# Performance work log

Measured on AMD Instinct MI355X. Metric: run time of the kernel, lower is better.

The kernel has to match this reference:

```python
import jax, jax.numpy as jnp
import numpy as np

B, L, D, H = 48, 512, 192, 6
DK = D // H
HID = 4 * D
EPS = 1e-5
SCALE = 1.0 / np.float32(np.sqrt(DK))


def _ln(x, g, b):
    mu = x.mean(-1, keepdims=True)
    v = ((x - mu) ** 2).mean(-1, keepdims=True)
    return (x - mu) * jax.lax.rsqrt(v + EPS) * g + b


def _mln(x, m, g, b):
    # masked layernorm: valid rows normalized, invalid rows pass through unchanged
    return jnp.where(m[..., None], _ln(x, g, b), x)


def _mha(q, k, v, mask, wq, bq, wk, bk, wv, bv, wo, bo):
    def proj(x, w, bb):
        return (x @ w + bb).reshape(B, L, H, DK).transpose(0, 2, 1, 3)  # [B,H,L,dk]
    Q, K, V = proj(q, wq, bq), proj(k, wk, bk), proj(v, wv, bv)
    s = jnp.einsum('bhqd,bhkd->bhqk', Q, K) * SCALE
    s = jnp.where(mask[:, None], -1e9, s)  # mask True = invalid pair
    p = jax.nn.softmax(s, axis=-1)
    o = jnp.einsum('bhqk,bhkd->bhqd', p, V).transpose(0, 2, 1, 3).reshape(B, L, D)
    return o @ wo + bo


def _forward(x_a, x_b, valid_a, valid_b,
             ln_a_g, ln_a_b, ln_b_g, ln_b_b, ln_oa_g, ln_oa_b, ln_ob_g, ln_ob_b,
             wq, bq, wk, bk, wv, bv, wo, bo,
             fln_g, fln_b, flno_g, flno_b, w1, b1, w2, b2):
    mB2A = ~(valid_a[:, :, None] & valid_b[:, None, :])  # [B,La,Lb]
    mA2B = ~(valid_b[:, :, None] & valid_a[:, None, :])
    a = _mln(x_a, valid_a, ln_a_g, ln_a_b)
    b = _mln(x_b, valid_b, ln_b_g, ln_b_b)
    oa = _mha(a, b, b, mB2A, wq, bq, wk, bk, wv, bv, wo, bo)
    oa = _mln(oa + x_a, valid_a, ln_oa_g, ln_oa_b)
    ob = _mha(b, a, a, mA2B, wq, bq, wk, bk, wv, bv, wo, bo)
    ob = _mln(ob + x_b, valid_b, ln_ob_g, ln_ob_b)

    def ffn(x, m):
        xn = _mln(x, m, fln_g, fln_b)
        y = jax.nn.gelu(xn @ w1 + b1, approximate=False) @ w2 + b2
        return _mln(x + y, m, flno_g, flno_b)

    return ffn(oa, valid_a), ffn(ob, valid_b)


def setup_inputs() -> dict:
    key = jax.random.key(0)
    ks = jax.random.split(key, 12)
    p = lambda k, s: jax.random.normal(k, s, dtype=jnp.float32) * 0.02
    ones = lambda s: jnp.ones(s, dtype=jnp.float32)
    zeros = lambda s: jnp.zeros(s, dtype=jnp.float32)
    return {
        'x_a': jax.random.normal(ks[0], (B, L, D), dtype=jnp.float32),
        'x_b': jax.random.normal(ks[1], (B, L, D), dtype=jnp.float32),
        'valid_a': jax.random.bernoulli(ks[2], 0.9, (B, L)),
        'valid_b': jax.random.bernoulli(ks[3], 0.9, (B, L)),
        'ln_a_g': ones((D,)), 'ln_a_b': zeros((D,)),
        'ln_b_g': ones((D,)), 'ln_b_b': zeros((D,)),
        'ln_oa_g': ones((D,)), 'ln_oa_b': zeros((D,)),
        'ln_ob_g': ones((D,)), 'ln_ob_b': zeros((D,)),
        'wq': p(ks[4], (D, D)), 'bq': zeros((D,)),
        'wk': p(ks[5], (D, D)), 'bk': zeros((D,)),
        'wv': p(ks[6], (D, D)), 'bv': zeros((D,)),
        'wo': p(ks[7], (D, D)), 'bo': zeros((D,)),
        'fln_g': ones((D,)), 'fln_b': zeros((D,)),
        'flno_g': ones((D,)), 'flno_b': zeros((D,)),
        'w1': p(ks[8], (D, HID)), 'b1': zeros((HID,)),
        'w2': p(ks[9], (HID, D)), 'b2': zeros((D,)),
    }


def reference(x_a, x_b, valid_a, valid_b,
              ln_a_g, ln_a_b, ln_b_g, ln_b_b, ln_oa_g, ln_oa_b, ln_ob_g, ln_ob_b,
              wq, bq, wk, bk, wv, bv, wo, bo,
              fln_g, fln_b, flno_g, flno_b, w1, b1, w2, b2):
    return _forward(x_a, x_b, valid_a, valid_b,
                    ln_a_g, ln_a_b, ln_b_g, ln_b_b, ln_oa_g, ln_oa_b, ln_ob_g, ln_ob_b,
                    wq, bq, wk, bk, wv, bv, wo, bo,
                    fln_g, fln_b, flno_g, flno_b, w1, b1, w2, b2)
```

## Files before the change

### kernel.cpp

```cpp
#include <hip/hip_runtime.h>
#include <math.h>

#define BB 48
#define LL 512
#define DD 192
#define HH 6
#define DKK 32
#define HID 768
#define ROWS (BB * LL)
#define BLD ((size_t)ROWS * DD)
#define SB2 0.25503531f
#define MASKED_X (-36.0f)

typedef unsigned short ushort_t;
typedef unsigned int uint_t;
typedef __bf16 bf16x8 __attribute__((ext_vector_type(8)));
typedef float f32x4 __attribute__((ext_vector_type(4)));

union U4BF8 { uint4 u; bf16x8 b; };
union BFU { __bf16 h; ushort_t u; };

__device__ __forceinline__ ushort_t f2bf(float f) {
  union { float f; uint_t u; } v; v.f = f;
  uint_t r = v.u + 0x7fffu + ((v.u >> 16) & 1u);
  return (ushort_t)(r >> 16);
}
__device__ __forceinline__ ushort_t cvt_bf(float f) {
  BFU c; c.h = (__bf16)f; return c.u;
}

__device__ __forceinline__ int swz_w(int n, int k, int N) {
  return ((k >> 5) * (N >> 4) + (n >> 4)) * 512 +
         ((((k & 31) >> 3) << 4) + (n & 15)) * 8 + (k & 7);
}

__global__ __launch_bounds__(256) void pack_kernel(
    const float* __restrict__ wq, const float* __restrict__ wk,
    const float* __restrict__ wv, const float* __restrict__ wo,
    const float* __restrict__ w1, const float* __restrict__ w2,
    const float* __restrict__ bq, const float* __restrict__ bk,
    const float* __restrict__ bv,
    ushort_t* __restrict__ Wqkv, ushort_t* __restrict__ Wo,
    ushort_t* __restrict__ W1, ushort_t* __restrict__ W2,
    float* __restrict__ bqkv) {
  int i = blockIdx.x * 256 + threadIdx.x;
  if (i < 110592) {
    int n2 = i / 192, k = i - n2 * 192;
    int part = n2 / 192, n = n2 - part * 192;
    const float* src = part == 0 ? wq : (part == 1 ? wk : wv);
    Wqkv[swz_w(n2, k, 576)] = f2bf(src[k * 192 + n]);
  } else if (i < 147456) {
    int j = i - 110592;
    int n = j / 192, k = j - n * 192;
    Wo[swz_w(n, k, 192)] = f2bf(wo[k * 192 + n]);
  } else if (i < 294912) {
    int j = i - 147456;
    int n = j / 192, k = j - n * 192;
    W1[j] = f2bf(w1[k * 768 + n]);
  } else if (i < 442368) {
    int j = i - 294912;
    int n = j / 768, k = j - n * 768;
    W2[j] = f2bf(w2[k * 192 + n]);
  } else if (i < 442944) {
    int j = i - 442368;
    bqkv[j] = j < 192 ? bq[j] : (j < 384 ? bk[j - 192] : bv[j - 384]);
  }
}

__global__ __launch_bounds__(256) void qkv_ln_kernel(
    const float* __restrict__ xa, const float* __restrict__ xb,
    const int* __restrict__ va, const int* __restrict__ vb,
    const float* __restrict__ g_a, const float* __restrict__ b_a,
    const float* __restrict__ g_b, const float* __restrict__ b_b,
    const ushort_t* __restrict__ Wsw, const float* __restrict__ bias,
    ushort_t* __restrict__ Cb) {
  constexpr int N = 576;
  constexpr int CSB = N + 8;
  __shared__ ushort_t smem[32 * CSB];
  ushort_t* As = smem;

  int tid = threadIdx.x;
  int w = tid >> 6, lane = tid & 63, l15 = lane & 15, kq = lane >> 4;
  int row0 = blockIdx.x * 32;
  int side = row0 >= ROWS;
  int rb = row0 - side * ROWS;

  {
    int row = tid >> 3, l8 = tid & 7;
    const float* xr = (side ? xb : xa) + (size_t)(rb + row) * DD + l8 * 24;
    float v[24];
    float s = 0.f;
#pragma unroll
    for (int j = 0; j < 6; ++j) {
      float4 q = *(const float4*)(xr + j * 4);
      v[j*4+0] = q.x; v[j*4+1] = q.y; v[j*4+2] = q.z; v[j*4+3] = q.w;
      s += q.x + q.y + q.z + q.w;
    }
    s += __shfl_xor(s, 1); s += __shfl_xor(s, 2); s += __shfl_xor(s, 4);
    float mu = s * (1.0f / 192.0f);
    float ss = 0.f;
#pragma unroll
    for (int j = 0; j < 24; ++j) { float d = v[j] - mu; ss += d * d; }
    ss += __shfl_xor(ss, 1); ss += __shfl_xor(ss, 2); ss += __shfl_xor(ss, 4);
    float inv = rsqrtf(ss * (1.0f / 192.0f) + 1e-5f);
    int vld = (side ? vb : va)[rb + row];
    const float* g = side ? g_b : g_a;
    const float* be = side ? b_b : b_a;
    ushort_t ob[24];
#pragma unroll
    for (int j = 0; j < 24; ++j) {
      int col = l8 * 24 + j;
      float r = vld ? (v[j] - mu) * inv * g[col] + be[col] : v[j];
      ob[j] = f2bf(r);
    }
#pragma unroll
    for (int j = 0; j < 3; ++j)
      *(uint4*)(&As[row * 200 + l8 * 24 + j * 8]) = *(const uint4*)(&ob[j * 8]);
  }
  __syncthreads();

  f32x4 acc[2][9];
#pragma unroll
  for (int qs = 0; qs < 2; ++qs)
#pragma unroll
    for (int nt = 0; nt < 9; ++nt) acc[qs][nt] = (f32x4){0.f, 0.f, 0.f, 0.f};

#pragma unroll 1
  for (int kk = 0; kk < 6; ++kk) {
    bf16x8 af[2];
#pragma unroll
    for (int qs = 0; qs < 2; ++qs)
      af[qs] = *(const bf16x8*)(&As[(qs * 16 + l15) * 200 + kk * 32 + kq * 8]);
    const ushort_t* wp =
        Wsw + ((size_t)(kk * (N >> 4) + w * 9) << 9) + lane * 8;
#pragma unroll
    for (int nt = 0; nt < 9; ++nt) {
      U4BF8 wf;
      wf.u = *(const uint4*)(wp + (nt << 9));
#pragma unroll
      for (int qs = 0; qs < 2; ++qs)
        acc[qs][nt] = __builtin_amdgcn_mfma_f32_16x16x32_bf16(
            af[qs], wf.b, acc[qs][nt], 0, 0, 0);
    }
  }
  __syncthreads();

  ushort_t* Cs = smem;
#pragma unroll
  for (int nt = 0; nt < 9; ++nt) {
    int col = (w * 9 + nt) * 16 + l15;
    float bb = bias[col];
#pragma unroll
    for (int qs = 0; qs < 2; ++qs)
#pragma unroll
      for (int r = 0; r < 4; ++r)
        Cs[(qs * 16 + kq * 4 + r) * CSB + col] = f2bf(acc[qs][nt][r] + bb);
  }
  __syncthreads();
  constexpr int UPR = (N * 2) / 16;
#pragma unroll
  for (int i = 0; i < (32 * UPR) / 256; ++i) {
    int idx = tid + i * 256;
    int r = idx / UPR, u = idx - r * UPR;
    *(uint4*)(Cb + (size_t)row0 * N + idx * 8) =
        *(const uint4*)(&Cs[r * CSB + u * 8]);
  }
}

__global__ __launch_bounds__(256) void oproj_ln_kernel(
    const ushort_t* __restrict__ A, const ushort_t* __restrict__ Wsw,
    const float* __restrict__ bias,
    const float* __restrict__ xa, const float* __restrict__ xb,
    const int* __restrict__ va, const int* __restrict__ vb,
    const float* __restrict__ g_oa, const float* __restrict__ b_oa,
    const float* __restrict__ g_ob, const float* __restrict__ b_ob,
    const float* __restrict__ g_f, const float* __restrict__ b_f,
    float* __restrict__ outf, ushort_t* __restrict__ outb) {
  __shared__ float smemf[32 * 196];
  ushort_t* As = (ushort_t*)smemf;

  int tid = threadIdx.x;
  int w = tid >> 6, lane = tid & 63, l15 = lane & 15, kq = lane >> 4;
  int row0 = blockIdx.x * 32;
  int side = row0 >= ROWS;
  int rb = row0 - side * ROWS;

  {
    const ushort_t* ap = A + (size_t)row0 * DD;
#pragma unroll
    for (int i = 0; i < 3; ++i) {
      int idx = tid + i * 256;
      int r = idx / 24, c = (idx - r * 24) * 8;
      *(uint4*)(&As[r * 200 + c]) = *(const uint4*)(ap + idx * 8);
    }
  }
  __syncthreads();

  f32x4 acc[2][3];
#pragma unroll
  for (int qs = 0; qs < 2; ++qs)
#pragma unroll
    for (int nt = 0; nt < 3; ++nt) acc[qs][nt] = (f32x4){0.f, 0.f, 0.f, 0.f};

#pragma unroll 1
  for (int kk = 0; kk < 6; ++kk) {
    bf16x8 af[2];
#pragma unroll
    for (int qs = 0; qs < 2; ++qs)
      af[qs] = *(const bf16x8*)(&As[(qs * 16 + l15) * 200 + kk * 32 + kq * 8]);
    const ushort_t* wp =
        Wsw + ((size_t)(kk * (192 >> 4) + w * 3) << 9) + lane * 8;
#pragma unroll
    for (int nt = 0; nt < 3; ++nt) {
      U4BF8 wf;
      wf.u = *(const uint4*)(wp + (nt << 9));
#pragma unroll
      for (int qs = 0; qs < 2; ++qs)
        acc[qs][nt] = __builtin_amdgcn_mfma_f32_16x16x32_bf16(
            af[qs], wf.b, acc[qs][nt], 0, 0, 0);
    }
  }
  __syncthreads();

  float* Cs = smemf;
#pragma unroll
  for (int nt = 0; nt < 3; ++nt) {
    int col = (w * 3 + nt) * 16 + l15;
    float bb = bias[col];
#pragma unroll
    for (int qs = 0; qs < 2; ++qs)
#pragma unroll
      for (int r = 0; r < 4; ++r)
        Cs[(qs * 16 + kq * 4 + r) * 196 + col] = acc[qs][nt][r] + bb;
  }
  __syncthreads();

  int row = tid >> 3, l8 = tid & 7;
  int grow = row0 + row;
  const float* xrow = (side ? xb : xa) + (size_t)(rb + row) * DD;
  const float* crow = &Cs[row * 196];
  float v[24];
  float s = 0.f;
#pragma unroll
  for (int j = 0; j < 6; ++j) {
    int col = j * 32 + l8 * 4;
    float4 q = *(const float4*)(xrow + col);
    v[j*4+0] = crow[col+0] + q.x; v[j*4+1] = crow[col+1] + q.y;
    v[j*4+2] = crow[col+2] + q.z; v[j*4+3] = crow[col+3] + q.w;
    s += v[j*4+0] + v[j*4+1] + v[j*4+2] + v[j*4+3];
  }
  s += __shfl_xor(s, 1); s += __shfl_xor(s, 2); s += __shfl_xor(s, 4);
  float mu = s * (1.0f / 192.0f);
  float ss = 0.f;
#pragma unroll
  for (int j = 0; j < 24; ++j) { float d = v[j] - mu; ss += d * d; }
  ss += __shfl_xor(ss, 1); ss += __shfl_xor(ss, 2); ss += __shfl_xor(ss, 4);
  float inv = rsqrtf(ss * (1.0f / 192.0f) + 1e-5f);
  int vld = (side ? vb : va)[rb + row];
  const float* g1 = side ? g_ob : g_oa;
  const float* b1 = side ? b_ob : b_oa;
  float y[24];
#pragma unroll
  for (int j = 0; j < 6; ++j) {
#pragma unroll
    for (int e = 0; e < 4; ++e) {
      int col = j * 32 + l8 * 4 + e;
      float vv = v[j * 4 + e];
      y[j * 4 + e] = vld ? (vv - mu) * inv * g1[col] + b1[col] : vv;
    }
  }
  float* orow = outf + (size_t)grow * DD;
#pragma unroll
  for (int j = 0; j < 6; ++j) {
    float4 q = {y[j*4+0], y[j*4+1], y[j*4+2], y[j*4+3]};
    *(float4*)(orow + j * 32 + l8 * 4) = q;
  }
  float s2 = 0.f;
#pragma unroll
  for (int j = 0; j < 24; ++j) s2 += y[j];
  s2 += __shfl_xor(s2, 1); s2 += __shfl_xor(s2, 2); s2 += __shfl_xor(s2, 4);
  float mu2 = s2 * (1.0f / 192.0f);
  float ss2 = 0.f;
#pragma unroll
  for (int j = 0; j < 24; ++j) { float e = y[j] - mu2; ss2 += e * e; }
  ss2 += __shfl_xor(ss2, 1); ss2 += __shfl_xor(ss2, 2); ss2 += __shfl_xor(ss2, 4);
  float inv2 = rsqrtf(ss2 * (1.0f / 192.0f) + 1e-5f);
  ushort_t* obrow = outb + (size_t)grow * DD;
#pragma unroll
  for (int j = 0; j < 6; ++j) {
    ushort_t zb[4];
#pragma unroll
    for (int e = 0; e < 4; ++e) {
      int col = j * 32 + l8 * 4 + e;
      float z = vld ? (y[j*4+e] - mu2) * inv2 * g_f[col] + b_f[col] : y[j*4+e];
      zb[e] = f2bf(z);
    }
    *(uint2*)(obrow + j * 32 + l8 * 4) = *(const uint2*)(&zb[0]);
  }
}

__global__ __launch_bounds__(256, 3) void ffn_fused_kernel(
    const ushort_t* __restrict__ A, const ushort_t* __restrict__ W1t,
    const float* __restrict__ bias1, const ushort_t* __restrict__ W2t,
    const float* __restrict__ bias2,
    const int* __restrict__ va, const int* __restrict__ vb,
    const float* __restrict__ g_f, const float* __restrict__ b_f,
    float* __restrict__ outf) {
  __shared__ float smemf[64 * 196];
  ushort_t* As = (ushort_t*)smemf;
  ushort_t* Hs = As + 64 * 200;

  int tid = threadIdx.x;
  int w = tid >> 6;
  int lane = tid & 63;
  int l15 = lane & 15;
  int kq = lane >> 4;
  int row0 = blockIdx.x * 64;
  int side = row0 >= ROWS;
  int rb0 = row0 - side * ROWS;

#pragma unroll
  for (int i = 0; i < 6; ++i) {
    int idx = tid + i * 256;
    int r = idx / 24, c = (idx % 24) * 8;
    *(uint4*)(&As[r * 200 + c]) = *(const uint4*)(A + (size_t)(row0 + r) * DD + c);
  }

  const ushort_t* w1p = W1t + (size_t)(w * 16 + l15) * DD + kq * 8;
  const ushort_t* w2p = W2t + (size_t)(w * 48 + l15) * HID + kq * 8;

  U4BF8 w1f[6], w1n[6], w2f[6];
#pragma unroll
  for (int kk = 0; kk < 6; ++kk)
    w1f[kk].u = *(const uint4*)(w1p + kk * 32);

  f32x4 Cacc[4][3];
#pragma unroll
  for (int qs = 0; qs < 4; ++qs)
#pragma unroll
    for (int nt = 0; nt < 3; ++nt) Cacc[qs][nt] = (f32x4){0.f, 0.f, 0.f, 0.f};

  __syncthreads();

  for (int hc = 0; hc < 12; ++hc) {
#pragma unroll
    for (int kk2 = 0; kk2 < 2; ++kk2)
#pragma unroll
      for (int nt = 0; nt < 3; ++nt)
        w2f[kk2 * 3 + nt].u =
            *(const uint4*)(w2p + (size_t)(nt * 16) * HID + hc * 64 + kk2 * 32);

    f32x4 Hacc[4];
#pragma unroll
    for (int qs = 0; qs < 4; ++qs) Hacc[qs] = (f32x4){0.f, 0.f, 0.f, 0.f};
#pragma unroll
    for (int kk = 0; kk < 6; ++kk) {
#pragma unroll
      for (int qs = 0; qs < 4; ++qs) {
        bf16x8 af = *(const bf16x8*)(&As[(qs * 16 + l15) * 200 + kk * 32 + kq * 8]);
        Hacc[qs] = __builtin_amdgcn_mfma_f32_16x16x32_bf16(
            af, w1f[kk].b, Hacc[qs], 0, 0, 0);
      }
    }

    if (hc < 11) {
#pragma unroll
      for (int kk = 0; kk < 6; ++kk)
        w1n[kk].u = *(const uint4*)(w1p + (size_t)(hc + 1) * 64 * DD + kk * 32);
    }

    {
      float bb = bias1[hc * 64 + w * 16 + l15];
      ushort_t* hb = &Hs[(hc & 1) * 4608];
#pragma unroll
      for (int qs = 0; qs < 4; ++qs)
#pragma unroll
        for (int r = 0; r < 4; ++r) {
          float x = Hacc[qs][r] + bb;
          x = 0.5f * x * (1.0f + erff(x * 0.70710678118654752f));
          hb[(qs * 16 + kq * 4 + r) * 72 + w * 16 + l15] = f2bf(x);
        }
    }
    __syncthreads();

#pragma unroll
    for (int kk2 = 0; kk2 < 2; ++kk2) {
      bf16x8 hf[4];
#pragma unroll
      for (int qs = 0; qs < 4; ++qs)
        hf[qs] = *(const bf16x8*)(&Hs[(hc & 1) * 4608 +
                                      (qs * 16 + l15) * 72 + kk2 * 32 + kq * 8]);
#pragma unroll
      for (int nt = 0; nt < 3; ++nt)
#pragma unroll
        for (int qs = 0; qs < 4; ++qs)
          Cacc[qs][nt] = __builtin_amdgcn_mfma_f32_16x16x32_bf16(
              hf[qs], w2f[kk2 * 3 + nt].b, Cacc[qs][nt], 0, 0, 0);
    }

#pragma unroll
    for (int kk = 0; kk < 6; ++kk) w1f[kk] = w1n[kk];
  }
  __syncthreads();

  float* Cs = smemf;
#pragma unroll
  for (int qs = 0; qs < 4; ++qs)
#pragma unroll
    for (int nt = 0; nt < 3; ++nt) {
      int col = w * 48 + nt * 16 + l15;
      float bb = bias2[col];
#pragma unroll
      for (int r = 0; r < 4; ++r)
        Cs[(qs * 16 + kq * 4 + r) * 196 + col] = Cacc[qs][nt][r] + bb;
    }
  __syncthreads();

  int row = tid >> 2, l4 = tid & 3;
  int grow = row0 + row;
  float* orow = outf + (size_t)grow * DD;
  const float* crow = &Cs[row * 196];
  float v[48];
  float s = 0.f;
#pragma unroll
  for (int j = 0; j < 12; ++j) {
    int col = j * 16 + l4 * 4;
    float4 q = *(const float4*)(orow + col);
    v[j*4+0] = crow[col+0] + q.x; v[j*4+1] = crow[col+1] + q.y;
    v[j*4+2] = crow[col+2] + q.z; v[j*4+3] = crow[col+3] + q.w;
    s += v[j*4+0] + v[j*4+1] + v[j*4+2] + v[j*4+3];
  }
  s += __shfl_xor(s, 1); s += __shfl_xor(s, 2);
  float mu = s * (1.0f / 192.0f);
  float ss = 0.f;
#pragma unroll
  for (int j = 0; j < 48; ++j) { float d = v[j] - mu; ss += d * d; }
  ss += __shfl_xor(ss, 1); ss += __shfl_xor(ss, 2);
  float inv = rsqrtf(ss * (1.0f / 192.0f) + 1e-5f);
  int vld = (side ? vb : va)[rb0 + row];
#pragma unroll
  for (int j = 0; j < 12; ++j) {
    int col = j * 16 + l4 * 4;
    float4 q;
#pragma unroll
    for (int e = 0; e < 4; ++e) {
      float vv = v[j * 4 + e];
      ((float*)&q)[e] = vld ? (vv - mu) * inv * g_f[col + e] + b_f[col + e] : vv;
    }
    *(float4*)(orow + col) = q;
  }
}

__global__ __launch_bounds__(256) void attn_mfma_kernel(
    const ushort_t* __restrict__ QKV,
    const int* __restrict__ valid_a, const int* __restrict__ valid_b,
    ushort_t* __restrict__ out) {
  int i = blockIdx.x;
  int gid = ((i >> 5) << 3) | (i & 7);
  int qt = (i >> 3) & 3;
  int side = gid >= BB * HH;
  int grem = side ? gid - BB * HH : gid;
  int h = grem % HH;
  int batch = grem / HH;
  int tid = threadIdx.x;
  int w = tid >> 6;
  int lane = tid & 63;
  int l15 = lane & 15;
  int kq = lane >> 4;

  const int* validq = side ? valid_b : valid_a;
  const int* validk = side ? valid_a : valid_b;
  size_t qrow0  = (size_t)side * ROWS + (size_t)batch * LL;
  size_t kvrow0 = (size_t)(1 - side) * ROWS + (size_t)batch * LL;

  __shared__ ushort_t VsT[32 * 72];
  __shared__ ushort_t Ps[4][32 * 72];

  int qbase = qt * 128 + w * 32;

  U4BF8 qfrag[2];
#pragma unroll
  for (int qs = 0; qs < 2; ++qs)
    qfrag[qs].u = *(const uint4*)(QKV + (qrow0 + qbase + qs * 16 + l15) * 576 +
                                  h * DKK + kq * 8);

  float sqf[2][4], mq[2][4];
#pragma unroll
  for (int qs = 0; qs < 2; ++qs)
#pragma unroll
    for (int r = 0; r < 4; ++r) {
      int vq = validq[batch * LL + qbase + qs * 16 + kq * 4 + r];
      sqf[qs][r] = vq ? SB2 : 0.0f;
      mq[qs][r]  = vq ? 0.0f : MASKED_X;
    }

  float lsum[2][4];
  f32x4 Oacc[2][2];
#pragma unroll
  for (int qs = 0; qs < 2; ++qs) {
#pragma unroll
    for (int r = 0; r < 4; ++r) lsum[qs][r] = 0.0f;
#pragma unroll
    for (int ds = 0; ds < 2; ++ds) Oacc[qs][ds] = (f32x4){0.f, 0.f, 0.f, 0.f};
  }

  for (int c = 0; c < LL; c += 64) {
    __syncthreads();
    uint4 vv = *(const uint4*)(QKV + (kvrow0 + c + lane) * 576 +
                               384 + h * DKK + w * 8);
    uint_t uu[4] = {vv.x, vv.y, vv.z, vv.w};
#pragma unroll
    for (int j = 0; j < 4; ++j) {
      VsT[(w * 8 + 2 * j) * 72 + lane]     = (ushort_t)(uu[j] & 0xffffu);
      VsT[(w * 8 + 2 * j + 1) * 72 + lane] = (ushort_t)(uu[j] >> 16);
    }
    __syncthreads();

    f32x4 S[2][4];
    float mkb[4];
#pragma unroll
    for (int ks = 0; ks < 4; ++ks) {
      U4BF8 kf;
      kf.u = *(const uint4*)(QKV + (kvrow0 + c + ks * 16 + l15) * 576 +
                             192 + h * DKK + kq * 8);
      mkb[ks] = validk[batch * LL + c + ks * 16 + l15] ? 0.0f : MASKED_X;
#pragma unroll
      for (int qs = 0; qs < 2; ++qs) {
        f32x4 z = (f32x4){0.f, 0.f, 0.f, 0.f};
        S[qs][ks] = __builtin_amdgcn_mfma_f32_16x16x32_bf16(
            qfrag[qs].b, kf.b, z, 0, 0, 0);
      }
    }

#pragma unroll
    for (int qs = 0; qs < 2; ++qs)
#pragma unroll
      for (int ks = 0; ks < 4; ++ks)
#pragma unroll
        for (int r = 0; r < 4; ++r) {
          float xs = fmaf(S[qs][ks][r], sqf[qs][r], fminf(mq[qs][r], mkb[ks]));
          float p = __builtin_amdgcn_exp2f(xs);
          lsum[qs][r] += p;
          Ps[w][(qs * 16 + kq * 4 + r) * 72 + ks * 16 + l15] = cvt_bf(p);
        }

#pragma unroll
    for (int kh = 0; kh < 2; ++kh) {
      bf16x8 pf[2], vf[2];
#pragma unroll
      for (int qs = 0; qs < 2; ++qs)
        pf[qs] = *(const bf16x8*)(&Ps[w][(qs * 16 + l15) * 72 + kh * 32 + kq * 8]);
#pragma unroll
      for (int ds = 0; ds < 2; ++ds)
        vf[ds] = *(const bf16x8*)(&VsT[(ds * 16 + l15) * 72 + kh * 32 + kq * 8]);
#pragma unroll
      for (int qs = 0; qs < 2; ++qs)
#pragma unroll
        for (int ds = 0; ds < 2; ++ds)
          Oacc[qs][ds] = __builtin_amdgcn_mfma_f32_16x16x32_bf16(
              pf[qs], vf[ds], Oacc[qs][ds], 0, 0, 0);
    }
  }

#pragma unroll
  for (int qs = 0; qs < 2; ++qs)
#pragma unroll
    for (int r = 0; r < 4; ++r) {
      float sm = lsum[qs][r];
#pragma unroll
      for (int off = 1; off < 16; off <<= 1) sm += __shfl_xor(sm, off);
      lsum[qs][r] = sm;
    }

#pragma unroll
  for (int qs = 0; qs < 2; ++qs)
#pragma unroll
    for (int ds = 0; ds < 2; ++ds)
#pragma unroll
      for (int r = 0; r < 4; ++r) {
        int q = qbase + qs * 16 + kq * 4 + r;
        out[(qrow0 + q) * DD + h * DKK + ds * 16 + l15] =
            f2bf(Oacc[qs][ds][r] / lsum[qs][r]);
      }
}

extern "C" void kernel_launch(void* const* d_in, const int* in_sizes, int n_in,
                              void* d_out, int out_size, void* d_ws, size_t ws_size,
                              hipStream_t stream) {
  const float* x_a = (const float*)d_in[0];
  const float* x_b = (const float*)d_in[1];
  const int* valid_a = (const int*)d_in[2];
  const int* valid_b = (const int*)d_in[3];
  const float* ln_a_g = (const float*)d_in[4];
  const float* ln_a_b = (const float*)d_in[5];
  const float* ln_b_g = (const float*)d_in[6];
  const float* ln_b_b = (const float*)d_in[7];
  const float* ln_oa_g = (const float*)d_in[8];
  const float* ln_oa_b = (const float*)d_in[9];
  const float* ln_ob_g = (const float*)d_in[10];
  const float* ln_ob_b = (const float*)d_in[11];
  const float* wq = (const float*)d_in[12];
  const float* bq = (const float*)d_in[13];
  const float* wk = (const float*)d_in[14];
  const float* bk = (const float*)d_in[15];
  const float* wv = (const float*)d_in[16];
  const float* bv = (const float*)d_in[17];
  const float* wo = (const float*)d_in[18];
  const float* bo = (const float*)d_in[19];
  const float* fln_g = (const float*)d_in[20];
  const float* fln_b = (const float*)d_in[21];
  const float* flno_g = (const float*)d_in[22];
  const float* flno_b = (const float*)d_in[23];
  const float* w1 = (const float*)d_in[24];
  const float* b1 = (const float*)d_in[25];
  const float* w2 = (const float*)d_in[26];
  const float* b2 = (const float*)d_in[27];

  char* wsb = (char*)d_ws;
  ushort_t* Wqkv = (ushort_t*)wsb;
  ushort_t* Wo_t = Wqkv + 110592;
  ushort_t* W1_t = Wo_t + 36864;
  ushort_t* W2_t = W1_t + 147456;
  float*    bqkv = (float*)(W2_t + 147456);
  ushort_t* lnFull = (ushort_t*)(wsb + 887040);
  ushort_t* attO   = lnFull;
  ushort_t* QKV = (ushort_t*)(wsb + 19761408);

  float* out_a = (float*)d_out;

  dim3 b256(256);
  dim3 gGemm(2 * ROWS / 32);
  dim3 gAttn(BB * HH * 4 * 2);
  dim3 gFFN(2 * ROWS / 64);

  hipLaunchKernelGGL(pack_kernel, dim3(1731), b256, 0, stream,
                     wq, wk, wv, wo, w1, w2, bq, bk, bv,
                     Wqkv, Wo_t, W1_t, W2_t, bqkv);

  hipLaunchKernelGGL(qkv_ln_kernel, gGemm, b256, 0, stream,
                     x_a, x_b, valid_a, valid_b,
                     ln_a_g, ln_a_b, ln_b_g, ln_b_b,
                     Wqkv, bqkv, QKV);

  hipLaunchKernelGGL(attn_mfma_kernel, gAttn, b256, 0, stream,
                     QKV, valid_a, valid_b, attO);

  hipLaunchKernelGGL(oproj_ln_kernel, gGemm, b256, 0, stream,
                     attO, Wo_t, bo, x_a, x_b, valid_a, valid_b,
                     ln_oa_g, ln_oa_b, ln_ob_g, ln_ob_b, fln_g, fln_b,
                     out_a, lnFull);

  hipLaunchKernelGGL(ffn_fused_kernel, gFFN, b256, 0, stream,
                     lnFull, W1_t, b1, W2_t, b2, valid_a, valid_b,
                     flno_g, flno_b, out_a);
}
```

Measured before the change: 364.5 us.

## Write V pre-transposed from QKV GEMM and read it directly in attention

The QKV projection now writes Q and K into a 384-wide buffer and stores V separately in a per-(side,batch,head) transposed layout [d][key]. The attention kernel then loads V fragments straight from global memory instead of staging and transposing V through shared memory each 64-key chunk, which removes two block barriers per iteration and the LDS transpose. In exchange, the GEMM epilogue does scattered 8-byte global stores for V, and attention issues more global loads per chunk that rely on cache hits.

New measurement: 391.1 us. 7.3% more time.

```diff
diff --git a/kernel.cpp b/kernel.cpp
--- a/kernel.cpp
+++ b/kernel.cpp
@@ -73,9 +73,9 @@
     const float* __restrict__ g_a, const float* __restrict__ b_a,
     const float* __restrict__ g_b, const float* __restrict__ b_b,
     const ushort_t* __restrict__ Wsw, const float* __restrict__ bias,
-    ushort_t* __restrict__ Cb) {
+    ushort_t* __restrict__ QK, ushort_t* __restrict__ Vt) {
   constexpr int N = 576;
-  constexpr int CSB = N + 8;
+  constexpr int CSB = 392;
   __shared__ ushort_t smem[32 * CSB];
   ushort_t* As = smem;
 
@@ -84,6 +84,8 @@
   int row0 = blockIdx.x * 32;
   int side = row0 >= ROWS;
   int rb = row0 - side * ROWS;
+  int batch = rb >> 9;
+  int k0 = rb & 511;
 
   {
     int row = tid >> 3, l8 = tid & 7;
@@ -148,21 +150,35 @@
   ushort_t* Cs = smem;
 #pragma unroll
   for (int nt = 0; nt < 9; ++nt) {
-    int col = (w * 9 + nt) * 16 + l15;
+    int t = w * 9 + nt;
+    int col = t * 16 + l15;
     float bb = bias[col];
-#pragma unroll
-    for (int qs = 0; qs < 2; ++qs)
-#pragma unroll
-      for (int r = 0; r < 4; ++r)
-        Cs[(qs * 16 + kq * 4 + r) * CSB + col] = f2bf(acc[qs][nt][r] + bb);
-  }
-  __syncthreads();
-  constexpr int UPR = (N * 2) / 16;
+    if (t < 24) {
+#pragma unroll
+      for (int qs = 0; qs < 2; ++qs)
+#pragma unroll
+        for (int r = 0; r < 4; ++r)
+          Cs[(qs * 16 + kq * 4 + r) * CSB + col] = f2bf(acc[qs][nt][r] + bb);
+    } else {
+      int vcol = col - 384;
+      int h = vcol >> 5, d = vcol & 31;
+      size_t vbase = ((size_t)((side * BB + batch) * HH + h) * 32 + d) * 512;
+#pragma unroll
+      for (int qs = 0; qs < 2; ++qs) {
+        ushort_t pk[4];
+#pragma unroll
+        for (int r = 0; r < 4; ++r) pk[r] = f2bf(acc[qs][nt][r] + bb);
+        *(uint2*)(Vt + vbase + k0 + qs * 16 + kq * 4) = *(const uint2*)(&pk[0]);
+      }
+    }
+  }
+  __syncthreads();
+  constexpr int UPR = 48;
 #pragma unroll
   for (int i = 0; i < (32 * UPR) / 256; ++i) {
     int idx = tid + i * 256;
     int r = idx / UPR, u = idx - r * UPR;
-    *(uint4*)(Cb + (size_t)row0 * N + idx * 8) =
+    *(uint4*)(QK + (size_t)row0 * 384 + idx * 8) =
         *(const uint4*)(&Cs[r * CSB + u * 8]);
   }
 }
@@ -452,7 +468,7 @@
 }
 
 __global__ __launch_bounds__(256) void attn_mfma_kernel(
-    const ushort_t* __restrict__ QKV,
+    const ushort_t* __restrict__ QK, const ushort_t* __restrict__ Vt,
     const int* __restrict__ valid_a, const int* __restrict__ valid_b,
     ushort_t* __restrict__ out) {
   int i = blockIdx.x;
@@ -472,8 +488,9 @@
   const int* validk = side ? valid_a : valid_b;
   size_t qrow0  = (size_t)side * ROWS + (size_t)batch * LL;
   size_t kvrow0 = (size_t)(1 - side) * ROWS + (size_t)batch * LL;
-
-  __shared__ ushort_t VsT[32 * 72];
+  const ushort_t* vtp =
+      Vt + ((size_t)(((1 - side) * BB + batch) * HH + h) * 32) * 512;
+
   __shared__ ushort_t Ps[4][32 * 72];
 
   int qbase = qt * 128 + w * 32;
@@ -481,7 +498,7 @@
   U4BF8 qfrag[2];
 #pragma unroll
   for (int qs = 0; qs < 2; ++qs)
-    qfrag[qs].u = *(const uint4*)(QKV + (qrow0 + qbase + qs * 16 + l15) * 576 +
+    qfrag[qs].u = *(const uint4*)(QK + (qrow0 + qbase + qs * 16 + l15) * 384 +
                                   h * DKK + kq * 8);
 
   float sqf[2][4], mq[2][4];
@@ -505,23 +522,12 @@
   }
 
   for (int c = 0; c < LL; c += 64) {
-    __syncthreads();
-    uint4 vv = *(const uint4*)(QKV + (kvrow0 + c + lane) * 576 +
-                               384 + h * DKK + w * 8);
-    uint_t uu[4] = {vv.x, vv.y, vv.z, vv.w};
-#pragma unroll
-    for (int j = 0; j < 4; ++j) {
-      VsT[(w * 8 + 2 * j) * 72 + lane]     = (ushort_t)(uu[j] & 0xffffu);
-      VsT[(w * 8 + 2 * j + 1) * 72 + lane] = (ushort_t)(uu[j] >> 16);
-    }
-    __syncthreads();
-
     f32x4 S[2][4];
     float mkb[4];
 #pragma unroll
     for (int ks = 0; ks < 4; ++ks) {
       U4BF8 kf;
-      kf.u = *(const uint4*)(QKV + (kvrow0 + c + ks * 16 + l15) * 576 +
+      kf.u = *(const uint4*)(QK + (kvrow0 + c + ks * 16 + l15) * 384 +
                              192 + h * DKK + kq * 8);
       mkb[ks] = validk[batch * LL + c + ks * 16 + l15] ? 0.0f : MASKED_X;
 #pragma unroll
@@ -552,7 +558,8 @@
         pf[qs] = *(const bf16x8*)(&Ps[w][(qs * 16 + l15) * 72 + kh * 32 + kq * 8]);
 #pragma unroll
       for (int ds = 0; ds < 2; ++ds)
-        vf[ds] = *(const bf16x8*)(&VsT[(ds * 16 + l15) * 72 + kh * 32 + kq * 8]);
+        vf[ds] = *(const bf16x8*)(vtp + (size_t)(ds * 16 + l15) * 512 +
+                                  c + kh * 32 + kq * 8);
 #pragma unroll
       for (int qs = 0; qs < 2; ++qs)
 #pragma unroll
@@ -624,7 +631,8 @@
   float*    bqkv = (float*)(W2_t + 147456);
   ushort_t* lnFull = (ushort_t*)(wsb + 887040);
   ushort_t* attO   = lnFull;
-  ushort_t* QKV = (ushort_t*)(wsb + 19761408);
+  ushort_t* QK = (ushort_t*)(wsb + 19761408);
+  ushort_t* Vt = (ushort_t*)(wsb + 57510144);
 
   float* out_a = (float*)d_out;
 
@@ -640,10 +648,10 @@
   hipLaunchKernelGGL(qkv_ln_kernel, gGemm, b256, 0, stream,
                      x_a, x_b, valid_a, valid_b,
                      ln_a_g, ln_a_b, ln_b_g, ln_b_b,
-                     Wqkv, bqkv, QKV);
+                     Wqkv, bqkv, QK, Vt);
 
   hipLaunchKernelGGL(attn_mfma_kernel, gAttn, b256, 0, stream,
-                     QKV, valid_a, valid_b, attO);
+                     QK, Vt, valid_a, valid_b, attO);
 
   hipLaunchKernelGGL(oproj_ln_kernel, gGemm, b256, 0, stream,
                      attO, Wo_t, bo, x_a, x_b, valid_a, valid_b,
```

## Double-buffer V tile and prefetch next K/V chunk in attention loop

Applied to the files above, without the earlier changes.

The attention kernel now double-buffers the transposed V tile in shared memory and prefetches the next chunk's K fragments, V row and key-valid flags into registers while the current chunk computes. This drops one __syncthreads per iteration and hides global load latency behind the MFMA and exp work. It also raises wave priority around the MFMA sections with s_setprio. The cost is extra registers and LDS, which may lower occupancy.

New measurement: 357.5 us (median of 2 runs). Within noise of the previous version (-1.9%).

```diff
diff --git a/kernel.cpp b/kernel.cpp
--- a/kernel.cpp
+++ b/kernel.cpp
@@ -473,7 +473,7 @@
   size_t qrow0  = (size_t)side * ROWS + (size_t)batch * LL;
   size_t kvrow0 = (size_t)(1 - side) * ROWS + (size_t)batch * LL;
 
-  __shared__ ushort_t VsT[32 * 72];
+  __shared__ ushort_t VsT[2][32 * 72];
   __shared__ ushort_t Ps[4][32 * 72];
 
   int qbase = qt * 128 + w * 32;
@@ -504,31 +504,56 @@
     for (int ds = 0; ds < 2; ++ds) Oacc[qs][ds] = (f32x4){0.f, 0.f, 0.f, 0.f};
   }
 
+  uint4 vv = *(const uint4*)(QKV + (kvrow0 + lane) * 576 + 384 + h * DKK + w * 8);
+  U4BF8 kf[4];
+  int vki[4];
+#pragma unroll
+  for (int ks = 0; ks < 4; ++ks) {
+    kf[ks].u = *(const uint4*)(QKV + (kvrow0 + ks * 16 + l15) * 576 +
+                               192 + h * DKK + kq * 8);
+    vki[ks] = validk[batch * LL + ks * 16 + l15];
+  }
+
   for (int c = 0; c < LL; c += 64) {
+    int buf = (c >> 6) & 1;
+    {
+      uint_t uu[4] = {vv.x, vv.y, vv.z, vv.w};
+#pragma unroll
+      for (int j = 0; j < 4; ++j) {
+        VsT[buf][(w * 8 + 2 * j) * 72 + lane]     = (ushort_t)(uu[j] & 0xffffu);
+        VsT[buf][(w * 8 + 2 * j + 1) * 72 + lane] = (ushort_t)(uu[j] >> 16);
+      }
+    }
+    uint4 vvn;
+    if (c + 64 < LL)
+      vvn = *(const uint4*)(QKV + (kvrow0 + c + 64 + lane) * 576 +
+                            384 + h * DKK + w * 8);
     __syncthreads();
-    uint4 vv = *(const uint4*)(QKV + (kvrow0 + c + lane) * 576 +
-                               384 + h * DKK + w * 8);
-    uint_t uu[4] = {vv.x, vv.y, vv.z, vv.w};
-#pragma unroll
-    for (int j = 0; j < 4; ++j) {
-      VsT[(w * 8 + 2 * j) * 72 + lane]     = (ushort_t)(uu[j] & 0xffffu);
-      VsT[(w * 8 + 2 * j + 1) * 72 + lane] = (ushort_t)(uu[j] >> 16);
-    }
-    __syncthreads();
 
     f32x4 S[2][4];
-    float mkb[4];
-#pragma unroll
-    for (int ks = 0; ks < 4; ++ks) {
-      U4BF8 kf;
-      kf.u = *(const uint4*)(QKV + (kvrow0 + c + ks * 16 + l15) * 576 +
-                             192 + h * DKK + kq * 8);
-      mkb[ks] = validk[batch * LL + c + ks * 16 + l15] ? 0.0f : MASKED_X;
+    __builtin_amdgcn_s_setprio(1);
+#pragma unroll
+    for (int ks = 0; ks < 4; ++ks)
 #pragma unroll
       for (int qs = 0; qs < 2; ++qs) {
         f32x4 z = (f32x4){0.f, 0.f, 0.f, 0.f};
         S[qs][ks] = __builtin_amdgcn_mfma_f32_16x16x32_bf16(
-            qfrag[qs].b, kf.b, z, 0, 0, 0);
+            qfrag[qs].b, kf[ks].b, z, 0, 0, 0);
+      }
+    __builtin_amdgcn_s_setprio(0);
+
+    float mkb[4];
+#pragma unroll
+    for (int ks = 0; ks < 4; ++ks) mkb[ks] = vki[ks] ? 0.0f : MASKED_X;
+
+    U4BF8 kfn[4];
+    int vkn[4];
+    if (c + 64 < LL) {
+#pragma unroll
+      for (int ks = 0; ks < 4; ++ks) {
+        kfn[ks].u = *(const uint4*)(QKV + (kvrow0 + c + 64 + ks * 16 + l15) * 576 +
+                                    192 + h * DKK + kq * 8);
+        vkn[ks] = validk[batch * LL + c + 64 + ks * 16 + l15];
       }
     }
 
@@ -544,6 +569,7 @@
           Ps[w][(qs * 16 + kq * 4 + r) * 72 + ks * 16 + l15] = cvt_bf(p);
         }
 
+    __builtin_amdgcn_s_setprio(1);
 #pragma unroll
     for (int kh = 0; kh < 2; ++kh) {
       bf16x8 pf[2], vf[2];
@@ -552,7 +578,7 @@
         pf[qs] = *(const bf16x8*)(&Ps[w][(qs * 16 + l15) * 72 + kh * 32 + kq * 8]);
 #pragma unroll
       for (int ds = 0; ds < 2; ++ds)
-        vf[ds] = *(const bf16x8*)(&VsT[(ds * 16 + l15) * 72 + kh * 32 + kq * 8]);
+        vf[ds] = *(const bf16x8*)(&VsT[buf][(ds * 16 + l15) * 72 + kh * 32 + kq * 8]);
 #pragma unroll
       for (int qs = 0; qs < 2; ++qs)
 #pragma unroll
@@ -560,6 +586,11 @@
           Oacc[qs][ds] = __builtin_amdgcn_mfma_f32_16x16x32_bf16(
               pf[qs], vf[ds], Oacc[qs][ds], 0, 0, 0);
     }
+    __builtin_amdgcn_s_setprio(0);
+
+    vv = vvn;
+#pragma unroll
+    for (int ks = 0; ks < 4; ++ks) { kf[ks] = kfn[ks]; vki[ks] = vkn[ks]; }
   }
 
 #pragma unroll
```
